# Kernel tuning notes

Hardware: AMD Instinct MI355X
Metric: run time of the kernel (lower is better)

## Reference

```python
import jax, jax.numpy as jnp
import numpy as np

MARGIN = 1.0


def setup_inputs() -> dict:
    key = jax.random.key(0)
    k1, k2, k3 = jax.random.split(key, 3)
    n, d = 8192, 128
    feat1 = jax.random.normal(k1, (n, d), dtype=jnp.float32)
    feat2 = jax.random.normal(k2, (n, d), dtype=jnp.float32)
    # similarity labels in {+1, -1}, as expected by HingeEmbeddingLoss
    simi = (2 * jax.random.randint(k3, (n, n), 0, 2) - 1).astype(jnp.int32)
    return {"feat1": feat1, "feat2": feat2, "simi": simi}


def reference(feat1, feat2, simi):
    # logits[i,j] = -||feat1_i - feat2_j||^2, computed without the O(n*m*d) expand
    sq1 = jnp.sum(feat1 * feat1, axis=-1, keepdims=True)          # [n, 1]
    sq2 = jnp.sum(feat2 * feat2, axis=-1)                          # [m]
    cross = jnp.einsum('nd,md->nm', feat1, feat2)                  # [n, m]
    logits = -(sq1 + sq2[None, :] - 2.0 * cross)                   # [n, m]
    probs = jax.nn.softmax(logits, axis=1)                         # [n, m]
    # HingeEmbeddingLoss: x if y==1 else max(0, margin - x); mean reduction
    loss = jnp.where(simi == 1, probs, jnp.maximum(0.0, MARGIN - probs))
    return jnp.mean(loss)
```

## Files before the change

kernel.cpp:

```cpp
#include <hip/hip_runtime.h>
#include <hip/hip_bf16.h>
#include <stdint.h>

#define N 8192
#define D 128
#define NCHUNK 8
#define CHUNK (N / NCHUNK)
#define RT 64
#define CT 64
#define NTILES (CHUNK / CT)

typedef short bf16x8 __attribute__((ext_vector_type(8)));
typedef float f32x4 __attribute__((ext_vector_type(4)));
typedef unsigned int uint32;

#define OFF_ACC   0u
#define OFF_SQ2   1024u
#define OFF_M     40960u
#define OFF_L     (OFF_M + NCHUNK * N * 4u)
#define OFF_S     (OFF_L + NCHUNK * N * 4u)
#define OFF_F1    (OFF_S + NCHUNK * N * 4u)
#define OFF_F2    (OFF_F1 + N * D * 2u)

__global__ void prep_kernel(const float* __restrict__ f1, const float* __restrict__ f2,
                            unsigned short* __restrict__ f1b, unsigned short* __restrict__ f2b,
                            float* __restrict__ sq2) {
    const int row = blockIdx.x;
    const int which = blockIdx.y;
    const int t = threadIdx.x;
    const float* src = which ? f2 : f1;
    unsigned short* dst = which ? f2b : f1b;
    float v0 = src[row * D + t];
    float v1 = src[row * D + t + 64];
    __hip_bfloat16 b0 = __float2bfloat16(v0);
    __hip_bfloat16 b1 = __float2bfloat16(v1);
    dst[row * D + t]      = *reinterpret_cast<unsigned short*>(&b0);
    dst[row * D + t + 64] = *reinterpret_cast<unsigned short*>(&b1);
    if (which) {
        float ss = v0 * v0 + v1 * v1;
        #pragma unroll
        for (int off = 32; off > 0; off >>= 1) ss += __shfl_xor(ss, off);
        if (t == 0) sq2[row] = ss;
    }
}

__global__ __launch_bounds__(256)
void main_kernel(const unsigned short* __restrict__ f1b,
                 const unsigned short* __restrict__ f2b,
                 const float* __restrict__ sq2,
                 const int* __restrict__ simi,
                 float* __restrict__ pm, float* __restrict__ pl, float* __restrict__ ps,
                 uint32* __restrict__ cnt_acc) {
    __shared__ unsigned short ldsB[CT * D];
    __shared__ float ldsSq[CHUNK];

    const int tid  = threadIdx.x;
    const int wave = tid >> 6;
    const int lane = tid & 63;
    const int lo   = lane & 15;
    const int hi   = lane >> 4;

    const int rowtile = blockIdx.x;
    const int chunk   = blockIdx.y;
    const int rbase   = rowtile * RT + wave * 16;
    const int cbase0  = chunk * CHUNK;

    for (int i = tid; i < CHUNK; i += 256) ldsSq[i] = sq2[cbase0 + i];

    bf16x8 afrag[4];
    {
        const unsigned short* ap = f1b + (rbase + lo) * D + hi * 8;
        #pragma unroll
        for (int kk = 0; kk < 4; kk++)
            afrag[kk] = *reinterpret_cast<const bf16x8*>(ap + kk * 32);
    }

    float m[4], l[4], s[4];
    #pragma unroll
    for (int r = 0; r < 4; r++) { m[r] = -1e30f; l[r] = 0.f; s[r] = 0.f; }
    uint32 cnt = 0;

    for (int t = 0; t < NTILES; t++) {
        const int cbase = cbase0 + t * CT;
        __syncthreads();
        #pragma unroll
        for (int it = 0; it < 4; it++) {
            int Lidx = it * 256 + tid;
            int row = Lidx >> 4, g = Lidx & 15;
            const uint4 v = *reinterpret_cast<const uint4*>(f2b + (cbase + row) * D + g * 8);
            *reinterpret_cast<uint4*>(ldsB + row * D + ((g ^ (row & 15)) * 8)) = v;
        }
        __syncthreads();

        int msk[4][4];
        #pragma unroll
        for (int cf = 0; cf < 4; cf++)
            #pragma unroll
            for (int r = 0; r < 4; r++)
                msk[cf][r] = simi[(long)(rbase + hi * 4 + r) * N + cbase + cf * 16 + lo];

        f32x4 acc[4];
        #pragma unroll
        for (int cf = 0; cf < 4; cf++) {
            acc[cf] = (f32x4){0.f, 0.f, 0.f, 0.f};
            const int brow = cf * 16 + lo;
            #pragma unroll
            for (int kk = 0; kk < 4; kk++) {
                int g = kk * 4 + hi;
                bf16x8 b = *reinterpret_cast<const bf16x8*>(
                    ldsB + brow * D + ((g ^ (brow & 15)) * 8));
                acc[cf] = __builtin_amdgcn_mfma_f32_16x16x32_bf16(afrag[kk], b, acc[cf], 0, 0, 0);
            }
        }

        float lg[4][4];
        float sqv[4];
        #pragma unroll
        for (int cf = 0; cf < 4; cf++) sqv[cf] = ldsSq[t * CT + cf * 16 + lo];
        #pragma unroll
        for (int cf = 0; cf < 4; cf++)
            #pragma unroll
            for (int r = 0; r < 4; r++)
                lg[cf][r] = 2.0f * acc[cf][r] - sqv[cf];

        #pragma unroll
        for (int r = 0; r < 4; r++) {
            float tm = fmaxf(fmaxf(lg[0][r], lg[1][r]), fmaxf(lg[2][r], lg[3][r]));
            #pragma unroll
            for (int off = 1; off < 16; off <<= 1)
                tm = fmaxf(tm, __shfl_xor(tm, off));
            float mn = fmaxf(m[r], tm);
            float al = __expf(m[r] - mn);
            l[r] *= al; s[r] *= al; m[r] = mn;
        }
        #pragma unroll
        for (int cf = 0; cf < 4; cf++)
            #pragma unroll
            for (int r = 0; r < 4; r++) {
                float p = __expf(lg[cf][r] - m[r]);
                l[r] += p;
                if (msk[cf][r] == 1) s[r] += p; else cnt++;
            }
    }

    #pragma unroll
    for (int r = 0; r < 4; r++) {
        #pragma unroll
        for (int off = 1; off < 16; off <<= 1) {
            l[r] += __shfl_xor(l[r], off);
            s[r] += __shfl_xor(s[r], off);
        }
    }
    if (lo == 0) {
        #pragma unroll
        for (int r = 0; r < 4; r++) {
            int row = rbase + hi * 4 + r;
            int idx = chunk * N + row;
            pm[idx] = m[r]; pl[idx] = l[r]; ps[idx] = s[r];
        }
    }
    #pragma unroll
    for (int off = 1; off < 64; off <<= 1) cnt += __shfl_xor(cnt, off);
    if (lane == 0) atomicAdd(cnt_acc, cnt);
}

__global__ void merge_kernel(const float* __restrict__ pm, const float* __restrict__ pl,
                             const float* __restrict__ ps, float* __restrict__ s_acc) {
    const int row = blockIdx.x * 256 + threadIdx.x;
    float M = -1e30f;
    #pragma unroll
    for (int k = 0; k < NCHUNK; k++) M = fmaxf(M, pm[k * N + row]);
    float L = 0.f, S = 0.f;
    #pragma unroll
    for (int k = 0; k < NCHUNK; k++) {
        float e = __expf(pm[k * N + row] - M);
        L += pl[k * N + row] * e;
        S += ps[k * N + row] * e;
    }
    float r = S / L;
    #pragma unroll
    for (int off = 32; off > 0; off >>= 1) r += __shfl_xor(r, off);
    __shared__ float red[4];
    int lane = threadIdx.x & 63, w = threadIdx.x >> 6;
    if (lane == 0) red[w] = r;
    __syncthreads();
    if (threadIdx.x == 0) atomicAdd(s_acc, red[0] + red[1] + red[2] + red[3]);
}

__global__ void final_kernel(const float* __restrict__ s_acc, const uint32* __restrict__ cnt_acc,
                             float* __restrict__ out) {
    double S = (double)s_acc[0];
    double C = (double)cnt_acc[0];
    double n = (double)N;
    out[0] = (float)((2.0 * S + C - n) / (n * n));
}

extern "C" void kernel_launch(void* const* d_in, const int* in_sizes, int n_in,
                              void* d_out, int out_size, void* d_ws, size_t ws_size,
                              hipStream_t stream) {
    const float* f1   = (const float*)d_in[0];
    const float* f2   = (const float*)d_in[1];
    const int*   simi = (const int*)d_in[2];
    float* out = (float*)d_out;
    char* ws = (char*)d_ws;

    float*  acc_s = (float*)(ws + OFF_ACC);
    uint32* acc_c = (uint32*)(ws + OFF_ACC + 4);
    float*  sq2   = (float*)(ws + OFF_SQ2);
    float*  pm    = (float*)(ws + OFF_M);
    float*  pl    = (float*)(ws + OFF_L);
    float*  ps    = (float*)(ws + OFF_S);
    unsigned short* f1b = (unsigned short*)(ws + OFF_F1);
    unsigned short* f2b = (unsigned short*)(ws + OFF_F2);

    hipMemsetAsync(ws + OFF_ACC, 0, 64, stream);
    prep_kernel<<<dim3(N, 2), 64, 0, stream>>>(f1, f2, f1b, f2b, sq2);
    main_kernel<<<dim3(N / RT, NCHUNK), 256, 0, stream>>>(f1b, f2b, sq2, simi, pm, pl, ps, acc_c);
    merge_kernel<<<N / 256, 256, 0, stream>>>(pm, pl, ps, acc_s);
    final_kernel<<<1, 1, 0, stream>>>(acc_s, acc_c, out);
}
```

Baseline: 443.8 us.

## Permute B columns so simi loads become int4 vectors; double chunk count

The B tile is loaded into LDS with a column permutation, so each lane's four MFMA output columns are four consecutive global columns. The simi mask can then be read as one int4 per row, and the mask loads are issued before the LDS barrier. NCHUNK rises to 16 for more blocks in the grid, launch bounds now request 8 waves per SIMD, and the prep kernel is rewritten as a grid-stride loop with one wave per row. The aim is fewer, wider, better-coalesced loads of the 256MB simi matrix, at the cost of more partial results to merge.

```diff
diff --git a/kernel.cpp b/kernel.cpp
--- a/kernel.cpp
+++ b/kernel.cpp
@@ -4,7 +4,7 @@
 
 #define N 8192
 #define D 128
-#define NCHUNK 8
+#define NCHUNK 16
 #define CHUNK (N / NCHUNK)
 #define RT 64
 #define CT 64
@@ -22,29 +22,30 @@
 #define OFF_F1    (OFF_S + NCHUNK * N * 4u)
 #define OFF_F2    (OFF_F1 + N * D * 2u)
 
-__global__ void prep_kernel(const float* __restrict__ f1, const float* __restrict__ f2,
-                            unsigned short* __restrict__ f1b, unsigned short* __restrict__ f2b,
-                            float* __restrict__ sq2) {
-    const int row = blockIdx.x;
-    const int which = blockIdx.y;
-    const int t = threadIdx.x;
-    const float* src = which ? f2 : f1;
-    unsigned short* dst = which ? f2b : f1b;
-    float v0 = src[row * D + t];
-    float v1 = src[row * D + t + 64];
-    __hip_bfloat16 b0 = __float2bfloat16(v0);
-    __hip_bfloat16 b1 = __float2bfloat16(v1);
-    dst[row * D + t]      = *reinterpret_cast<unsigned short*>(&b0);
-    dst[row * D + t + 64] = *reinterpret_cast<unsigned short*>(&b1);
-    if (which) {
-        float ss = v0 * v0 + v1 * v1;
+__global__ __launch_bounds__(256)
+void prep_kernel(const float* __restrict__ f1, const float* __restrict__ f2,
+                 unsigned short* __restrict__ f1b, unsigned short* __restrict__ f2b,
+                 float* __restrict__ sq2) {
+    const int w    = blockIdx.x * 4 + (threadIdx.x >> 6);
+    const int lane = threadIdx.x & 63;
+    for (int row = w; row < N; row += 1024) {
+        float a0 = f1[row * D + lane];
+        float a1 = f1[row * D + 64 + lane];
+        float b0 = f2[row * D + lane];
+        float b1 = f2[row * D + 64 + lane];
+        __hip_bfloat16 t;
+        t = __float2bfloat16(a0); f1b[row * D + lane]      = *(unsigned short*)&t;
+        t = __float2bfloat16(a1); f1b[row * D + 64 + lane] = *(unsigned short*)&t;
+        t = __float2bfloat16(b0); f2b[row * D + lane]      = *(unsigned short*)&t;
+        t = __float2bfloat16(b1); f2b[row * D + 64 + lane] = *(unsigned short*)&t;
+        float ss = b0 * b0 + b1 * b1;
         #pragma unroll
         for (int off = 32; off > 0; off >>= 1) ss += __shfl_xor(ss, off);
-        if (t == 0) sq2[row] = ss;
-    }
-}
-
-__global__ __launch_bounds__(256)
+        if (lane == 0) sq2[row] = ss;
+    }
+}
+
+__global__ __launch_bounds__(256, 8)
 void main_kernel(const unsigned short* __restrict__ f1b,
                  const unsigned short* __restrict__ f2b,
                  const float* __restrict__ sq2,
@@ -75,6 +76,11 @@
             afrag[kk] = *reinterpret_cast<const bf16x8*>(ap + kk * 32);
     }
 
+    const int sq_ = (tid >> 4);
+    const int sg_ = tid & 15;
+
+    const int* simi_p = simi + (size_t)(rbase + hi * 4) * N + cbase0 + 4 * lo;
+
     float m[4], l[4], s[4];
     #pragma unroll
     for (int r = 0; r < 4; r++) { m[r] = -1e30f; l[r] = 0.f; s[r] = 0.f; }
@@ -82,22 +88,21 @@
 
     for (int t = 0; t < NTILES; t++) {
         const int cbase = cbase0 + t * CT;
+
+        int4 msk[4];
+        #pragma unroll
+        for (int r = 0; r < 4; r++)
+            msk[r] = *reinterpret_cast<const int4*>(simi_p + (size_t)r * N);
+
         __syncthreads();
         #pragma unroll
         for (int it = 0; it < 4; it++) {
-            int Lidx = it * 256 + tid;
-            int row = Lidx >> 4, g = Lidx & 15;
-            const uint4 v = *reinterpret_cast<const uint4*>(f2b + (cbase + row) * D + g * 8);
-            *reinterpret_cast<uint4*>(ldsB + row * D + ((g ^ (row & 15)) * 8)) = v;
+            int q = it * 16 + sq_;
+            int c = 4 * (q & 15) + (q >> 4);
+            const uint4 v = *reinterpret_cast<const uint4*>(f2b + (size_t)(cbase + c) * D + sg_ * 8);
+            *reinterpret_cast<uint4*>(ldsB + q * D + ((sg_ ^ (q & 15)) * 8)) = v;
         }
         __syncthreads();
-
-        int msk[4][4];
-        #pragma unroll
-        for (int cf = 0; cf < 4; cf++)
-            #pragma unroll
-            for (int r = 0; r < 4; r++)
-                msk[cf][r] = simi[(long)(rbase + hi * 4 + r) * N + cbase + cf * 16 + lo];
 
         f32x4 acc[4];
         #pragma unroll
@@ -113,10 +118,9 @@
             }
         }
 
+        f32x4 sqv = *reinterpret_cast<const f32x4*>(&ldsSq[t * CT + 4 * lo]);
+
         float lg[4][4];
-        float sqv[4];
-        #pragma unroll
-        for (int cf = 0; cf < 4; cf++) sqv[cf] = ldsSq[t * CT + cf * 16 + lo];
         #pragma unroll
         for (int cf = 0; cf < 4; cf++)
             #pragma unroll
@@ -134,13 +138,16 @@
             l[r] *= al; s[r] *= al; m[r] = mn;
         }
         #pragma unroll
-        for (int cf = 0; cf < 4; cf++)
-            #pragma unroll
-            for (int r = 0; r < 4; r++) {
+        for (int r = 0; r < 4; r++) {
+            const int mk[4] = {msk[r].x, msk[r].y, msk[r].z, msk[r].w};
+            #pragma unroll
+            for (int cf = 0; cf < 4; cf++) {
                 float p = __expf(lg[cf][r] - m[r]);
                 l[r] += p;
-                if (msk[cf][r] == 1) s[r] += p; else cnt++;
+                if (mk[cf] == 1) s[r] += p; else cnt++;
             }
+        }
+        simi_p += CT;
     }
 
     #pragma unroll
@@ -214,7 +221,7 @@
     unsigned short* f2b = (unsigned short*)(ws + OFF_F2);
 
     hipMemsetAsync(ws + OFF_ACC, 0, 64, stream);
-    prep_kernel<<<dim3(N, 2), 64, 0, stream>>>(f1, f2, f1b, f2b, sq2);
+    prep_kernel<<<256, 256, 0, stream>>>(f1, f2, f1b, f2b, sq2);
     main_kernel<<<dim3(N / RT, NCHUNK), 256, 0, stream>>>(f1b, f2b, sq2, simi, pm, pl, ps, acc_c);
     merge_kernel<<<N / 256, 256, 0, stream>>>(pm, pl, ps, acc_s);
     final_kernel<<<1, 1, 0, stream>>>(acc_s, acc_c, out);
```

Result: slower. 533.0 us (+20.1%).
